# Optimization experiments

Hardware: AMD Instinct MI355X
Metric: run time of the kernel (lower is better)

## Reference

```python
import jax, jax.numpy as jnp
import numpy as np

N = 50000
E = 800000
F_IN = 256
H = 64      # hidden_channels
NH = 4      # GAT heads

def setup_inputs() -> dict:
    key = jax.random.key(0)
    ks = jax.random.split(key, 16)
    x = jax.random.normal(ks[0], (N, F_IN), dtype=jnp.float32)
    edge_index = jax.random.randint(ks[1], (2, E), 0, N, dtype=jnp.int64)
    def w(k, shape, fan_in):
        return jax.random.normal(k, shape, dtype=jnp.float32) / np.sqrt(fan_in)
    return {
        "x": x, "edge_index": edge_index,
        "W1": w(ks[2], (F_IN, H), F_IN), "b1": jnp.zeros((H,), jnp.float32),
        "W2": w(ks[3], (H, H), H),       "b2": jnp.zeros((H,), jnp.float32),
        "Wg": w(ks[4], (H, NH * H), H),
        "att_src": w(ks[5], (NH, H), H), "att_dst": w(ks[6], (NH, H), H),
        "bg": jnp.zeros((NH * H,), jnp.float32),
        "Wf1": w(ks[7], (NH * H, H), NH * H), "bf1": jnp.zeros((H,), jnp.float32),
        "Wf2": w(ks[8], (H, 1), H),           "bf2": jnp.zeros((1,), jnp.float32),
    }

def _with_self_loops(edge_index):
    loops = jnp.arange(N, dtype=edge_index.dtype)
    src = jnp.concatenate([edge_index[0], loops])
    dst = jnp.concatenate([edge_index[1], loops])
    return src, dst

def _gcn(h, src, dst, W, b):
    # h: [N, d_in] -> [N, d_out]; symmetric norm D^-1/2 (A+I) D^-1/2
    h = h @ W
    deg = jax.ops.segment_sum(jnp.ones_like(dst, dtype=h.dtype), dst, num_segments=N)
    dinv = jnp.where(deg > 0, jax.lax.rsqrt(deg), 0.0)
    norm = dinv[src] * dinv[dst]                      # [E2]
    out = jax.ops.segment_sum(h[src] * norm[:, None], dst, num_segments=N)
    return out + b

def _gat(h, src, dst, Wg, att_src, att_dst, bg):
    hp = (h @ Wg).reshape(N, NH, H)                   # [N, NH, H]
    a_src = jnp.einsum('nhd,hd->nh', hp, att_src)     # [N, NH]
    a_dst = jnp.einsum('nhd,hd->nh', hp, att_dst)
    alpha = jax.nn.leaky_relu(a_src[src] + a_dst[dst], negative_slope=0.2)  # [E2, NH]
    amax = jax.ops.segment_max(alpha, dst, num_segments=N)
    e = jnp.exp(alpha - amax[dst])
    denom = jax.ops.segment_sum(e, dst, num_segments=N)
    coef = e / denom[dst]                             # [E2, NH]
    out = jax.ops.segment_sum(hp[src] * coef[:, :, None], dst, num_segments=N)
    return out.reshape(N, NH * H) + bg

def reference(x, edge_index, W1, b1, W2, b2, Wg, att_src, att_dst, bg, Wf1, bf1, Wf2, bf2):
    src, dst = _with_self_loops(edge_index)
    h = jax.nn.relu(_gcn(x, src, dst, W1, b1))        # dropout inactive (eval)
    h = jax.nn.relu(_gcn(h, src, dst, W2, b2))
    h = _gat(h, src, dst, Wg, att_src, att_dst, bg)
    h = jax.nn.relu(h @ Wf1 + bf1)
    return h @ Wf2 + bf2                              # [N, 1]
```

## Files before the change

### kernel.cpp

```cpp
#include <hip/hip_runtime.h>
#include <hip/hip_fp16.h>
#include <math.h>


#define CAP 64
#define CAPSH 6
#define BSH 8
#define NBKT 256
#define BCAP 8192

typedef _Float16 v4h __attribute__((ext_vector_type(4)));
typedef float v4f __attribute__((ext_vector_type(4)));

__device__ __forceinline__ float lrelu02(float a) { return fmaxf(a, 0.2f * a); }

__device__ __forceinline__ float4 lrelu4(float4 a) {
    return make_float4(lrelu02(a.x), lrelu02(a.y), lrelu02(a.z), lrelu02(a.w));
}

__device__ __forceinline__ float4 exp4(float4 a) {
    return make_float4(__expf(a.x), __expf(a.y), __expf(a.z), __expf(a.w));
}

__device__ __forceinline__ float4 unpack4(float2 raw) {
    __half2 h01 = *(__half2*)&raw.x;
    __half2 h23 = *(__half2*)&raw.y;
    float2 f01 = __half22float2(h01);
    float2 f23 = __half22float2(h23);
    return make_float4(f01.x, f01.y, f23.x, f23.y);
}

__device__ __forceinline__ float2 pack4(float4 v) {
    float2 r;
    *(__half2*)&r.x = __float22half2_rn(make_float2(v.x, v.y));
    *(__half2*)&r.y = __float22half2_rn(make_float2(v.z, v.w));
    return r;
}


__launch_bounds__(256)
__global__ void k_bucket(const int* __restrict__ src, const int* __restrict__ dst, int E,
                         int* __restrict__ bcnt, unsigned int* __restrict__ stage) {
    __shared__ int hist[NBKT];
    __shared__ int base[NBKT];
    __shared__ int cur[NBKT];
    int t = threadIdx.x;
    hist[t] = 0; cur[t] = 0;
    __syncthreads();
    int base_e = blockIdx.x * 2048;
    int d[8], s[8];
#pragma unroll
    for (int i = 0; i < 8; i++) {
        int e = base_e + t + i * 256;
        bool ok = (e < E);
        d[i] = ok ? dst[e] : -1;
        s[i] = ok ? src[e] : 0;
        if (ok) atomicAdd(&hist[d[i] >> BSH], 1);
    }
    __syncthreads();
    if (hist[t] > 0) base[t] = atomicAdd(&bcnt[t], hist[t]);
    __syncthreads();
#pragma unroll
    for (int i = 0; i < 8; i++) {
        if (d[i] >= 0) {
            int b = d[i] >> BSH;
            int p = base[b] + atomicAdd(&cur[b], 1);
            if (p < BCAP)
                stage[(size_t)b * BCAP + p] = ((unsigned)d[i] << 16) | (unsigned)s[i];
        }
    }
}


__launch_bounds__(256)
__global__ void k_scatter2(const unsigned int* __restrict__ stage,
                           const int* __restrict__ bcnt, int* __restrict__ cnt,
                           unsigned short* __restrict__ slots, int n) {
    __shared__ int lcnt[1 << BSH];
    int t = threadIdx.x;
    int k = blockIdx.x;
    lcnt[t] = 0;
    __syncthreads();
    int ne = bcnt[k];
    if (ne > BCAP) ne = BCAP;
    const unsigned int* st = stage + (size_t)k * BCAP;
    for (int i = t; i < ne; i += 256) {
        unsigned int e = st[i];
        int d = e >> 16;
        int p = atomicAdd(&lcnt[d & ((1 << BSH) - 1)], 1);
        if (p < CAP) slots[((size_t)d << CAPSH) + p] = (unsigned short)(e & 0xFFFF);
    }
    __syncthreads();
    int v = (k << BSH) + t;
    if (v < n) cnt[v] = lcnt[t];
}


#define GEMM_BODY(BX, K, COLS)                                                     \
    __shared__ float As[16][68];                                                   \
    __shared__ float Bs[16][68];                                                   \
    const int row0 = (BX) * 64;                                                    \
    const int col0 = blockIdx.y * 64;                                              \
    const int t = threadIdx.x;                                                     \
    const int tx = t & 15;                                                         \
    const int ty = t >> 4;                                                         \
    const int lm = t >> 2;                                                         \
    const int lk4 = (t & 3) << 2;                                                  \
    const int wk = t >> 4;                                                         \
    const int wc = (t & 15) << 2;                                                  \
    float acc[4][4] = {};                                                          \
    for (int k0 = 0; k0 < K; k0 += 16) {                                           \
        float4 av = make_float4(0.f, 0.f, 0.f, 0.f);                               \
        int r = row0 + lm;                                                         \
        if (r < nrows) av = *(const float4*)(X + (size_t)r * K + k0 + lk4);        \
        As[lk4 + 0][lm] = av.x;                                                    \
        As[lk4 + 1][lm] = av.y;                                                    \
        As[lk4 + 2][lm] = av.z;                                                    \
        As[lk4 + 3][lm] = av.w;                                                    \
        *(float4*)&Bs[wk][wc] = *(const float4*)(W + (size_t)(k0 + wk) * COLS + col0 + wc); \
        __syncthreads();                                                           \
        _Pragma("unroll") for (int kk = 0; kk < 16; kk++) {                        \
            float4 a = *(const float4*)&As[kk][ty << 2];                           \
            float4 b = *(const float4*)&Bs[kk][tx << 2];                           \
            acc[0][0] = fmaf(a.x, b.x, acc[0][0]);                                 \
            acc[0][1] = fmaf(a.x, b.y, acc[0][1]);                                 \
            acc[0][2] = fmaf(a.x, b.z, acc[0][2]);                                 \
            acc[0][3] = fmaf(a.x, b.w, acc[0][3]);                                 \
            acc[1][0] = fmaf(a.y, b.x, acc[1][0]);                                 \
            acc[1][1] = fmaf(a.y, b.y, acc[1][1]);                                 \
            acc[1][2] = fmaf(a.y, b.z, acc[1][2]);                                 \
            acc[1][3] = fmaf(a.y, b.w, acc[1][3]);                                 \
            acc[2][0] = fmaf(a.z, b.x, acc[2][0]);                                 \
            acc[2][1] = fmaf(a.z, b.y, acc[2][1]);                                 \
            acc[2][2] = fmaf(a.z, b.z, acc[2][2]);                                 \
            acc[2][3] = fmaf(a.z, b.w, acc[2][3]);                                 \
            acc[3][0] = fmaf(a.w, b.x, acc[3][0]);                                 \
            acc[3][1] = fmaf(a.w, b.y, acc[3][1]);                                 \
            acc[3][2] = fmaf(a.w, b.z, acc[3][2]);                                 \
            acc[3][3] = fmaf(a.w, b.w, acc[3][3]);                                 \
        }                                                                          \
        __syncthreads();                                                           \
    }

__launch_bounds__(256)
__global__ void k_fused1(const int* __restrict__ cnt,
                         const float* __restrict__ X, const float* __restrict__ W,
                         __half* __restrict__ Y, int nrows, int gemmBlocks,
                         const float* __restrict__ Wg, const float* __restrict__ att_src,
                         const float* __restrict__ att_dst, const float* __restrict__ Wf1,
                         const float* __restrict__ bf1, const float* __restrict__ bg,
                         const float* __restrict__ W2, float* __restrict__ watt,
                         __half* __restrict__ WcF, __half* __restrict__ W2F,
                         float* __restrict__ bias2) {
    if ((int)blockIdx.x >= gemmBlocks) {
        int b2 = blockIdx.x - gemmBlocks;
        int tt = threadIdx.x;
        if (b2 < 64) {
            int idx = b2 * 256 + tt;
            int r = idx >> 6, c = idx & 63;
            int h = r >> 6, k = r & 63;
            float s = 0.f;
            for (int j = 0; j < 64; j++)
                s = fmaf(Wg[k * 256 + h * 64 + j], Wf1[(h * 64 + j) * 64 + c], s);
            int ks = r >> 4, kr = r & 15;
            int lfrag = ((kr >> 2) << 4) | (c & 15);
            int jf = kr & 3;
            int w = c >> 4;
            WcF[((((w << 4) | ks) << 6) | lfrag) * 4 + jf] = __float2half_rn(s);
        } else {
            for (int idx = tt; idx < 512; idx += 256) {
                int k = idx >> 3, c8 = idx & 7;
                int h = c8 & 3;
                const float* att = (c8 < 4) ? att_src : att_dst;
                float s = 0.f;
                for (int c = 0; c < 64; c++)
                    s = fmaf(Wg[k * 256 + h * 64 + c], att[h * 64 + c], s);
                watt[k * 8 + c8] = s;
            }
            if (tt < 64) {
                float s = bf1[tt];
                for (int j = 0; j < 256; j++) s = fmaf(bg[j], Wf1[j * 64 + tt], s);
                bias2[tt] = s;
            }
            for (int f = tt; f < 4096; f += 256) {
                int jf = f & 3, lfrag = (f >> 2) & 63, ws = f >> 8;
                int w = ws >> 2, ks = ws & 3;
                int k = ks * 16 + ((lfrag >> 4) << 2) + jf;
                int c = w * 16 + (lfrag & 15);
                W2F[f] = __float2half_rn(W2[k * 64 + c]);
            }
        }
        return;
    }
    GEMM_BODY(blockIdx.x, 256, 64)
#pragma unroll
    for (int i = 0; i < 4; i++) {
        int row = row0 + (ty << 2) + i;
        if (row >= nrows) break;
        float dv = rsqrtf((float)(min(cnt[row], CAP) + 1));
        float4 o = make_float4(acc[i][0] * dv, acc[i][1] * dv,
                               acc[i][2] * dv, acc[i][3] * dv);
        ((float2*)(Y + (size_t)row * 64))[tx] = pack4(o);
    }
}


__launch_bounds__(256)
__global__ void k_gcn1_gemm2(const __half* __restrict__ A, const unsigned short* __restrict__ slots,
                             const int* __restrict__ cnt, const float* __restrict__ b1,
                             const __half* __restrict__ W2F, __half* __restrict__ A2, int n) {
    __shared__ alignas(16) __half s_oh[16 * 68];
    __shared__ alignas(16) __half s_res[16 * 68];
    __shared__ float s_dv[16];
    int t = threadIdx.x;
    int lane = t & 63;
    int l = t & 15;
    int nb = t >> 4;
    int v = blockIdx.x * 16 + nb;
    bool act = (v < n);
    if (act) {
        int deg = min(cnt[v], CAP);
        const unsigned short* lst = slots + ((size_t)v << CAPSH);
        float dv = rsqrtf((float)(deg + 1));
        float4 a0 = unpack4(((const float2*)(A + (size_t)v * 64))[l]);
        float4 a1 = make_float4(0.f, 0.f, 0.f, 0.f);
        float4 a2 = a1, a3 = a1;
        int j = 0;
        for (; j + 7 < deg; j += 8) {
            ushort4 sa = *(const ushort4*)(lst + j);
            ushort4 sb = *(const ushort4*)(lst + j + 4);
            float4 t0 = unpack4(((const float2*)(A + (size_t)sa.x * 64))[l]);
            float4 t1 = unpack4(((const float2*)(A + (size_t)sa.y * 64))[l]);
            float4 t2 = unpack4(((const float2*)(A + (size_t)sa.z * 64))[l]);
            float4 t3 = unpack4(((const float2*)(A + (size_t)sa.w * 64))[l]);
            float4 t4 = unpack4(((const float2*)(A + (size_t)sb.x * 64))[l]);
            float4 t5 = unpack4(((const float2*)(A + (size_t)sb.y * 64))[l]);
            float4 t6 = unpack4(((const float2*)(A + (size_t)sb.z * 64))[l]);
            float4 t7 = unpack4(((const float2*)(A + (size_t)sb.w * 64))[l]);
            a0.x += t0.x + t4.x; a0.y += t0.y + t4.y; a0.z += t0.z + t4.z; a0.w += t0.w + t4.w;
            a1.x += t1.x + t5.x; a1.y += t1.y + t5.y; a1.z += t1.z + t5.z; a1.w += t1.w + t5.w;
            a2.x += t2.x + t6.x; a2.y += t2.y + t6.y; a2.z += t2.z + t6.z; a2.w += t2.w + t6.w;
            a3.x += t3.x + t7.x; a3.y += t3.y + t7.y; a3.z += t3.z + t7.z; a3.w += t3.w + t7.w;
        }
        for (; j + 3 < deg; j += 4) {
            ushort4 sa = *(const ushort4*)(lst + j);
            float4 t0 = unpack4(((const float2*)(A + (size_t)sa.x * 64))[l]);
            float4 t1 = unpack4(((const float2*)(A + (size_t)sa.y * 64))[l]);
            float4 t2 = unpack4(((const float2*)(A + (size_t)sa.z * 64))[l]);
            float4 t3 = unpack4(((const float2*)(A + (size_t)sa.w * 64))[l]);
            a0.x += t0.x; a0.y += t0.y; a0.z += t0.z; a0.w += t0.w;
            a1.x += t1.x; a1.y += t1.y; a1.z += t1.z; a1.w += t1.w;
            a2.x += t2.x; a2.y += t2.y; a2.z += t2.z; a2.w += t2.w;
            a3.x += t3.x; a3.y += t3.y; a3.z += t3.z; a3.w += t3.w;
        }
        for (; j < deg; j++) {
            float4 ta = unpack4(((const float2*)(A + (size_t)lst[j] * 64))[l]);
            a0.x += ta.x; a0.y += ta.y; a0.z += ta.z; a0.w += ta.w;
        }
        a0.x += a1.x + a2.x + a3.x;
        a0.y += a1.y + a2.y + a3.y;
        a0.z += a1.z + a2.z + a3.z;
        a0.w += a1.w + a2.w + a3.w;
        float4 b = ((const float4*)b1)[l];
        float4 o;
        o.x = fmaxf(fmaf(dv, a0.x, b.x), 0.f);
        o.y = fmaxf(fmaf(dv, a0.y, b.y), 0.f);
        o.z = fmaxf(fmaf(dv, a0.z, b.z), 0.f);
        o.w = fmaxf(fmaf(dv, a0.w, b.w), 0.f);
        *(float2*)&s_oh[nb * 68 + (l << 2)] = pack4(o);
        if (l == 0) s_dv[nb] = dv;
    } else {
        *(float2*)&s_oh[nb * 68 + (l << 2)] = make_float2(0.f, 0.f);
        if (l == 0) s_dv[nb] = 0.f;
    }
    __syncthreads();
    int w = t >> 6;
    v4f acc = {0.f, 0.f, 0.f, 0.f};
    int arow = (lane & 15) * 68;
    int acol = (lane >> 4) << 2;
#pragma unroll
    for (int ks = 0; ks < 4; ks++) {
        v4h a = *(const v4h*)&s_oh[arow + ks * 16 + acol];
        v4h bfr = *(const v4h*)&W2F[((((w << 2) | ks) << 6) | lane) << 2];
        acc = __builtin_amdgcn_mfma_f32_16x16x16f16(a, bfr, acc, 0, 0, 0);
    }
    int cc = (w << 4) | (lane & 15);
    int m0 = (lane >> 4) << 2;
#pragma unroll
    for (int j = 0; j < 4; j++)
        s_res[(m0 + j) * 68 + cc] = __float2half_rn(acc[j] * s_dv[m0 + j]);
    __syncthreads();
    if (act)
        ((float2*)(A2 + (size_t)v * 64))[l] = *(const float2*)&s_res[nb * 68 + (l << 2)];
}


__launch_bounds__(256)
__global__ void k_gcn2_att(const __half* __restrict__ T, const unsigned short* __restrict__ slots,
                           const int* __restrict__ cnt, const float* __restrict__ bias,
                           const float* __restrict__ watt, __half* __restrict__ Out,
                           float* __restrict__ asrc, float* __restrict__ adst, int n) {
    int t = threadIdx.x;
    int l = t & 15;
    int v = blockIdx.x * 16 + (t >> 4);
    if (v >= n) return;
    int deg = min(cnt[v], CAP);
    const unsigned short* lst = slots + ((size_t)v << CAPSH);
    float dv = rsqrtf((float)(deg + 1));
    float4 a0 = unpack4(((const float2*)(T + (size_t)v * 64))[l]);
    float4 a1 = make_float4(0.f, 0.f, 0.f, 0.f);
    float4 a2 = a1, a3 = a1;
    int j = 0;
    for (; j + 7 < deg; j += 8) {
        ushort4 sa = *(const ushort4*)(lst + j);
        ushort4 sb = *(const ushort4*)(lst + j + 4);
        float4 t0 = unpack4(((const float2*)(T + (size_t)sa.x * 64))[l]);
        float4 t1 = unpack4(((const float2*)(T + (size_t)sa.y * 64))[l]);
        float4 t2 = unpack4(((const float2*)(T + (size_t)sa.z * 64))[l]);
        float4 t3 = unpack4(((const float2*)(T + (size_t)sa.w * 64))[l]);
        float4 t4 = unpack4(((const float2*)(T + (size_t)sb.x * 64))[l]);
        float4 t5 = unpack4(((const float2*)(T + (size_t)sb.y * 64))[l]);
        float4 t6 = unpack4(((const float2*)(T + (size_t)sb.z * 64))[l]);
        float4 t7 = unpack4(((const float2*)(T + (size_t)sb.w * 64))[l]);
        a0.x += t0.x + t4.x; a0.y += t0.y + t4.y; a0.z += t0.z + t4.z; a0.w += t0.w + t4.w;
        a1.x += t1.x + t5.x; a1.y += t1.y + t5.y; a1.z += t1.z + t5.z; a1.w += t1.w + t5.w;
        a2.x += t2.x + t6.x; a2.y += t2.y + t6.y; a2.z += t2.z + t6.z; a2.w += t2.w + t6.w;
        a3.x += t3.x + t7.x; a3.y += t3.y + t7.y; a3.z += t3.z + t7.z; a3.w += t3.w + t7.w;
    }
    for (; j + 3 < deg; j += 4) {
        ushort4 sa = *(const ushort4*)(lst + j);
        float4 t0 = unpack4(((const float2*)(T + (size_t)sa.x * 64))[l]);
        float4 t1 = unpack4(((const float2*)(T + (size_t)sa.y * 64))[l]);
        float4 t2 = unpack4(((const float2*)(T + (size_t)sa.z * 64))[l]);
        float4 t3 = unpack4(((const float2*)(T + (size_t)sa.w * 64))[l]);
        a0.x += t0.x; a0.y += t0.y; a0.z += t0.z; a0.w += t0.w;
        a1.x += t1.x; a1.y += t1.y; a1.z += t1.z; a1.w += t1.w;
        a2.x += t2.x; a2.y += t2.y; a2.z += t2.z; a2.w += t2.w;
        a3.x += t3.x; a3.y += t3.y; a3.z += t3.z; a3.w += t3.w;
    }
    for (; j < deg; j++) {
        float4 ta = unpack4(((const float2*)(T + (size_t)lst[j] * 64))[l]);
        a0.x += ta.x; a0.y += ta.y; a0.z += ta.z; a0.w += ta.w;
    }
    a0.x += a1.x + a2.x + a3.x;
    a0.y += a1.y + a2.y + a3.y;
    a0.z += a1.z + a2.z + a3.z;
    a0.w += a1.w + a2.w + a3.w;
    float4 b = ((const float4*)bias)[l];
    float4 o;
    o.x = fmaxf(fmaf(dv, a0.x, b.x), 0.f);
    o.y = fmaxf(fmaf(dv, a0.y, b.y), 0.f);
    o.z = fmaxf(fmaf(dv, a0.z, b.z), 0.f);
    o.w = fmaxf(fmaf(dv, a0.w, b.w), 0.f);
    ((float2*)(Out + (size_t)v * 64))[l] = pack4(o);
    const float* wr = watt + (l << 2) * 8;
    float4 w0a = *(const float4*)(wr +  0), w0b = *(const float4*)(wr +  4);
    float4 w1a = *(const float4*)(wr +  8), w1b = *(const float4*)(wr + 12);
    float4 w2a = *(const float4*)(wr + 16), w2b = *(const float4*)(wr + 20);
    float4 w3a = *(const float4*)(wr + 24), w3b = *(const float4*)(wr + 28);
    float4 ds, dd;
    ds.x = o.x*w0a.x + o.y*w1a.x + o.z*w2a.x + o.w*w3a.x;
    ds.y = o.x*w0a.y + o.y*w1a.y + o.z*w2a.y + o.w*w3a.y;
    ds.z = o.x*w0a.z + o.y*w1a.z + o.z*w2a.z + o.w*w3a.z;
    ds.w = o.x*w0a.w + o.y*w1a.w + o.z*w2a.w + o.w*w3a.w;
    dd.x = o.x*w0b.x + o.y*w1b.x + o.z*w2b.x + o.w*w3b.x;
    dd.y = o.x*w0b.y + o.y*w1b.y + o.z*w2b.y + o.w*w3b.y;
    dd.z = o.x*w0b.z + o.y*w1b.z + o.z*w2b.z + o.w*w3b.z;
    dd.w = o.x*w0b.w + o.y*w1b.w + o.z*w2b.w + o.w*w3b.w;
    for (int off = 1; off <= 8; off <<= 1) {
        ds.x += __shfl_xor(ds.x, off); ds.y += __shfl_xor(ds.y, off);
        ds.z += __shfl_xor(ds.z, off); ds.w += __shfl_xor(ds.w, off);
        dd.x += __shfl_xor(dd.x, off); dd.y += __shfl_xor(dd.y, off);
        dd.z += __shfl_xor(dd.z, off); dd.w += __shfl_xor(dd.w, off);
    }
    if (l == 0) {
        ((float4*)asrc)[v] = ds;
        ((float4*)adst)[v] = dd;
    }
}


__launch_bounds__(256)
__global__ void k_gat_head(const __half* __restrict__ Bt, const unsigned short* __restrict__ slots,
                           const int* __restrict__ cnt, const float* __restrict__ asrc,
                           const float* __restrict__ adst, const __half* __restrict__ WcF,
                           const float* __restrict__ bias2, const float* __restrict__ Wf2,
                           const float* __restrict__ bf2, float* __restrict__ out, int n) {
    __shared__ alignas(16) __half s_aggh[16 * 260];
    __shared__ alignas(16) float s_e[16 * 68];
    __shared__ int s_sidx[16 * 17];
    __shared__ float s_part[16][4];
    int t = threadIdx.x;
    int lane = t & 63;
    int l = lane & 15;
    int nb = t >> 4;
    int v = blockIdx.x * 16 + nb;
    bool act = (v < n);
    if (act) {
        int deg = min(cnt[v], CAP);
        const unsigned short* lst = slots + ((size_t)v << CAPSH);
        float4 ad4 = ((const float4*)adst)[v];
        float4 as4 = ((const float4*)asrc)[v];
        float4 es = exp4(lrelu4(make_float4(as4.x + ad4.x, as4.y + ad4.y,
                                            as4.z + ad4.z, as4.w + ad4.w)));
        float4 esum = (l == 0) ? es : make_float4(0.f, 0.f, 0.f, 0.f);
        float4 bv = unpack4(((const float2*)(Bt + (size_t)v * 64))[l]);
        float4 acc0 = make_float4(es.x * bv.x, es.x * bv.y, es.x * bv.z, es.x * bv.w);
        float4 acc1 = make_float4(es.y * bv.x, es.y * bv.y, es.y * bv.z, es.y * bv.w);
        float4 acc2 = make_float4(es.z * bv.x, es.z * bv.y, es.z * bv.z, es.z * bv.w);
        float4 acc3 = make_float4(es.w * bv.x, es.w * bv.y, es.w * bv.z, es.w * bv.w);
        for (int c0 = 0; c0 < deg; c0 += 16) {
            int cl = min(16, deg - c0);
            float4 e = make_float4(0.f, 0.f, 0.f, 0.f);
            if (l < cl) {
                int s = lst[c0 + l];
                float4 sa = ((const float4*)asrc)[s];
                e = exp4(lrelu4(make_float4(sa.x + ad4.x, sa.y + ad4.y,
                                            sa.z + ad4.z, sa.w + ad4.w)));
                esum.x += e.x; esum.y += e.y; esum.z += e.z; esum.w += e.w;
                s_sidx[nb * 17 + l] = s;
            }
            *(float4*)&s_e[nb * 68 + (l << 2)] = e;
            __builtin_amdgcn_sched_barrier(0);
            for (int jj = 0; jj < cl; jj++) {
                int so = s_sidx[nb * 17 + jj];
                float4 ev = *(const float4*)&s_e[nb * 68 + (jj << 2)];
                float4 tv = unpack4(((const float2*)(Bt + (size_t)so * 64))[l]);
                acc0.x = fmaf(ev.x, tv.x, acc0.x); acc0.y = fmaf(ev.x, tv.y, acc0.y);
                acc0.z = fmaf(ev.x, tv.z, acc0.z); acc0.w = fmaf(ev.x, tv.w, acc0.w);
                acc1.x = fmaf(ev.y, tv.x, acc1.x); acc1.y = fmaf(ev.y, tv.y, acc1.y);
                acc1.z = fmaf(ev.y, tv.z, acc1.z); acc1.w = fmaf(ev.y, tv.w, acc1.w);
                acc2.x = fmaf(ev.z, tv.x, acc2.x); acc2.y = fmaf(ev.z, tv.y, acc2.y);
                acc2.z = fmaf(ev.z, tv.z, acc2.z); acc2.w = fmaf(ev.z, tv.w, acc2.w);
                acc3.x = fmaf(ev.w, tv.x, acc3.x); acc3.y = fmaf(ev.w, tv.y, acc3.y);
                acc3.z = fmaf(ev.w, tv.z, acc3.z); acc3.w = fmaf(ev.w, tv.w, acc3.w);
            }
        }
        for (int o = 8; o >= 1; o >>= 1) {
            esum.x += __shfl_xor(esum.x, o); esum.y += __shfl_xor(esum.y, o);
            esum.z += __shfl_xor(esum.z, o); esum.w += __shfl_xor(esum.w, o);
        }
        float i0 = 1.f / esum.x, i1 = 1.f / esum.y, i2 = 1.f / esum.z, i3 = 1.f / esum.w;
        *(float2*)&s_aggh[nb * 260 +   0 + (l << 2)] =
            pack4(make_float4(acc0.x*i0, acc0.y*i0, acc0.z*i0, acc0.w*i0));
        *(float2*)&s_aggh[nb * 260 +  64 + (l << 2)] =
            pack4(make_float4(acc1.x*i1, acc1.y*i1, acc1.z*i1, acc1.w*i1));
        *(float2*)&s_aggh[nb * 260 + 128 + (l << 2)] =
            pack4(make_float4(acc2.x*i2, acc2.y*i2, acc2.z*i2, acc2.w*i2));
        *(float2*)&s_aggh[nb * 260 + 192 + (l << 2)] =
            pack4(make_float4(acc3.x*i3, acc3.y*i3, acc3.z*i3, acc3.w*i3));
    } else {
        float2 z = make_float2(0.f, 0.f);
        *(float2*)&s_aggh[nb * 260 +   0 + (l << 2)] = z;
        *(float2*)&s_aggh[nb * 260 +  64 + (l << 2)] = z;
        *(float2*)&s_aggh[nb * 260 + 128 + (l << 2)] = z;
        *(float2*)&s_aggh[nb * 260 + 192 + (l << 2)] = z;
    }
    __syncthreads();
    int w = t >> 6;
    v4f accA = {0.f, 0.f, 0.f, 0.f};
    v4f accB = {0.f, 0.f, 0.f, 0.f};
    int arow = l * 260;
    int acol = (lane >> 4) << 2;
#pragma unroll
    for (int ks = 0; ks < 16; ks += 2) {
        v4h a0f = *(const v4h*)&s_aggh[arow + ks * 16 + acol];
        v4h b0f = *(const v4h*)&WcF[((((w << 4) | ks) << 6) | lane) << 2];
        accA = __builtin_amdgcn_mfma_f32_16x16x16f16(a0f, b0f, accA, 0, 0, 0);
        v4h a1f = *(const v4h*)&s_aggh[arow + (ks + 1) * 16 + acol];
        v4h b1f = *(const v4h*)&WcF[((((w << 4) | (ks + 1)) << 6) | lane) << 2];
        accB = __builtin_amdgcn_mfma_f32_16x16x16f16(a1f, b1f, accB, 0, 0, 0);
    }
    int cc = (w << 4) | l;
    float bb = bias2[cc], wq = Wf2[cc];
    float p0 = fmaxf(accA[0] + accB[0] + bb, 0.f) * wq;
    float p1 = fmaxf(accA[1] + accB[1] + bb, 0.f) * wq;
    float p2 = fmaxf(accA[2] + accB[2] + bb, 0.f) * wq;
    float p3 = fmaxf(accA[3] + accB[3] + bb, 0.f) * wq;
    for (int o = 1; o <= 8; o <<= 1) {
        p0 += __shfl_xor(p0, o); p1 += __shfl_xor(p1, o);
        p2 += __shfl_xor(p2, o); p3 += __shfl_xor(p3, o);
    }
    if (l == 0) {
        int m0 = (lane >> 4) << 2;
        s_part[m0 + 0][w] = p0; s_part[m0 + 1][w] = p1;
        s_part[m0 + 2][w] = p2; s_part[m0 + 3][w] = p3;
    }
    __syncthreads();
    if (t < 16 && blockIdx.x * 16 + t < n)
        out[blockIdx.x * 16 + t] =
            s_part[t][0] + s_part[t][1] + s_part[t][2] + s_part[t][3] + bf2[0];
}


extern "C" void kernel_launch(void* const* d_in, const int* in_sizes, int n_in,
                              void* d_out, int out_size, void* d_ws, size_t ws_size,
                              hipStream_t stream) {
    const float* x       = (const float*)d_in[0];
    const int*   ei      = (const int*)d_in[1];
    const float* W1      = (const float*)d_in[2];
    const float* b1      = (const float*)d_in[3];
    const float* W2      = (const float*)d_in[4];
    const float* b2      = (const float*)d_in[5];
    const float* Wg      = (const float*)d_in[6];
    const float* att_src = (const float*)d_in[7];
    const float* att_dst = (const float*)d_in[8];
    const float* bg      = (const float*)d_in[9];
    const float* Wf1     = (const float*)d_in[10];
    const float* bf1     = (const float*)d_in[11];
    const float* Wf2     = (const float*)d_in[12];
    const float* bf2     = (const float*)d_in[13];
    float* out = (float*)d_out;

    const int N = in_sizes[0] / 256;
    const int E = in_sizes[1] / 2;
    const int* src = ei;
    const int* dst = ei + E;

    char* p = (char*)d_ws;
    auto alloc = [&](size_t bytes) {
        void* r = (void*)p;
        p += (bytes + 255) & ~(size_t)255;
        return r;
    };
    __half* A   = (__half*)alloc((size_t)N * 64 * 2);
    __half* A2  = (__half*)alloc((size_t)N * 64 * 2);
    __half* B   = (__half*)alloc((size_t)N * 64 * 2);
    float* asrc = (float*)alloc((size_t)N * 4 * 4);
    float* adst = (float*)alloc((size_t)N * 4 * 4);
    int*   cnt  = (int*)alloc((size_t)N * 4);
    unsigned short* slots = (unsigned short*)alloc((size_t)N * CAP * 2);
    int* bcnt = (int*)alloc(NBKT * 4);
    unsigned int* stage = (unsigned int*)alloc((size_t)NBKT * BCAP * 4);
    float* watt   = (float*)alloc(64 * 8 * 4);
    __half* WcF   = (__half*)alloc(256 * 64 * 2);
    __half* W2F   = (__half*)alloc(64 * 64 * 2);
    float* bias2  = (float*)alloc(64 * 4);

    const int gBkt = (E + 2047) / 2048;
    const int nbused = (N + (1 << BSH) - 1) >> BSH;
    const int grow = (N + 63) / 64;
    const int gagg = (N + 15) / 16;

    hipMemsetAsync(bcnt, 0, NBKT * 4, stream);

    k_bucket<<<gBkt, 256, 0, stream>>>(src, dst, E, bcnt, stage);

    k_scatter2<<<nbused, 256, 0, stream>>>(stage, bcnt, cnt, slots, N);

    k_fused1<<<grow + 65, 256, 0, stream>>>(
        cnt, x, W1, A, N, grow,
        Wg, att_src, att_dst, Wf1, bf1, bg, W2, watt, WcF, W2F, bias2);

    k_gcn1_gemm2<<<gagg, 256, 0, stream>>>(A, slots, cnt, b1, W2F, A2, N);

    k_gcn2_att<<<gagg, 256, 0, stream>>>(A2, slots, cnt, b2, watt, B, asrc, adst, N);

    k_gat_head<<<gagg, 256, 0, stream>>>(B, slots, cnt, asrc, adst,
                                         WcF, bias2, Wf2, bf2, out, N);
}
```

Before: 237.7 us.

## Replace FP32 SIMT first-layer GEMM with fp16 MFMA using prepacked W1 fragments

The first GCN linear layer (X @ W1, 50000x256x64) moves from a scalar FP32 shared-memory tiled GEMM to MFMA 16x16x16 fp16 instructions. W1 is converted to fp16 and laid out in MFMA B-fragment order by one extra block added to the bucketing kernel. X tiles are converted to fp16 in shared memory, and results go through a shared-memory staging buffer for coalesced 16-byte stores. The aim is to cut compute time in this GEMM, which is likely bound by reading the 51 MB X. Rounding X and W1 to fp16 lowers input precision.

Result: faster. 225.3 us (-5.2%).

```diff
diff --git a/kernel.cpp b/kernel.cpp
--- a/kernel.cpp
+++ b/kernel.cpp
@@ -40,7 +40,19 @@
 
 __launch_bounds__(256)
 __global__ void k_bucket(const int* __restrict__ src, const int* __restrict__ dst, int E,
-                         int* __restrict__ bcnt, unsigned int* __restrict__ stage) {
+                         int* __restrict__ bcnt, unsigned int* __restrict__ stage,
+                         int nBktBlocks, const float* __restrict__ W1,
+                         __half* __restrict__ W1F) {
+    if ((int)blockIdx.x >= nBktBlocks) {
+        for (int f = threadIdx.x; f < 16384; f += 256) {
+            int jf = f & 3, lane = (f >> 2) & 63, ws = f >> 8;
+            int w = ws >> 4, ks = ws & 15;
+            int k = ks * 16 + ((lane >> 4) << 2) + jf;
+            int c = (w << 4) | (lane & 15);
+            W1F[f] = __float2half_rn(W1[k * 64 + c]);
+        }
+        return;
+    }
     __shared__ int hist[NBKT];
     __shared__ int base[NBKT];
     __shared__ int cur[NBKT];
@@ -96,55 +108,9 @@
 }
 
 
-#define GEMM_BODY(BX, K, COLS)                                                     \
-    __shared__ float As[16][68];                                                   \
-    __shared__ float Bs[16][68];                                                   \
-    const int row0 = (BX) * 64;                                                    \
-    const int col0 = blockIdx.y * 64;                                              \
-    const int t = threadIdx.x;                                                     \
-    const int tx = t & 15;                                                         \
-    const int ty = t >> 4;                                                         \
-    const int lm = t >> 2;                                                         \
-    const int lk4 = (t & 3) << 2;                                                  \
-    const int wk = t >> 4;                                                         \
-    const int wc = (t & 15) << 2;                                                  \
-    float acc[4][4] = {};                                                          \
-    for (int k0 = 0; k0 < K; k0 += 16) {                                           \
-        float4 av = make_float4(0.f, 0.f, 0.f, 0.f);                               \
-        int r = row0 + lm;                                                         \
-        if (r < nrows) av = *(const float4*)(X + (size_t)r * K + k0 + lk4);        \
-        As[lk4 + 0][lm] = av.x;                                                    \
-        As[lk4 + 1][lm] = av.y;                                                    \
-        As[lk4 + 2][lm] = av.z;                                                    \
-        As[lk4 + 3][lm] = av.w;                                                    \
-        *(float4*)&Bs[wk][wc] = *(const float4*)(W + (size_t)(k0 + wk) * COLS + col0 + wc); \
-        __syncthreads();                                                           \
-        _Pragma("unroll") for (int kk = 0; kk < 16; kk++) {                        \
-            float4 a = *(const float4*)&As[kk][ty << 2];                           \
-            float4 b = *(const float4*)&Bs[kk][tx << 2];                           \
-            acc[0][0] = fmaf(a.x, b.x, acc[0][0]);                                 \
-            acc[0][1] = fmaf(a.x, b.y, acc[0][1]);                                 \
-            acc[0][2] = fmaf(a.x, b.z, acc[0][2]);                                 \
-            acc[0][3] = fmaf(a.x, b.w, acc[0][3]);                                 \
-            acc[1][0] = fmaf(a.y, b.x, acc[1][0]);                                 \
-            acc[1][1] = fmaf(a.y, b.y, acc[1][1]);                                 \
-            acc[1][2] = fmaf(a.y, b.z, acc[1][2]);                                 \
-            acc[1][3] = fmaf(a.y, b.w, acc[1][3]);                                 \
-            acc[2][0] = fmaf(a.z, b.x, acc[2][0]);                                 \
-            acc[2][1] = fmaf(a.z, b.y, acc[2][1]);                                 \
-            acc[2][2] = fmaf(a.z, b.z, acc[2][2]);                                 \
-            acc[2][3] = fmaf(a.z, b.w, acc[2][3]);                                 \
-            acc[3][0] = fmaf(a.w, b.x, acc[3][0]);                                 \
-            acc[3][1] = fmaf(a.w, b.y, acc[3][1]);                                 \
-            acc[3][2] = fmaf(a.w, b.z, acc[3][2]);                                 \
-            acc[3][3] = fmaf(a.w, b.w, acc[3][3]);                                 \
-        }                                                                          \
-        __syncthreads();                                                           \
-    }
-
 __launch_bounds__(256)
 __global__ void k_fused1(const int* __restrict__ cnt,
-                         const float* __restrict__ X, const float* __restrict__ W,
+                         const float* __restrict__ X, const __half* __restrict__ W1F,
                          __half* __restrict__ Y, int nrows, int gemmBlocks,
                          const float* __restrict__ Wg, const float* __restrict__ att_src,
                          const float* __restrict__ att_dst, const float* __restrict__ Wf1,
@@ -192,15 +158,70 @@
         }
         return;
     }
-    GEMM_BODY(blockIdx.x, 256, 64)
-#pragma unroll
-    for (int i = 0; i < 4; i++) {
-        int row = row0 + (ty << 2) + i;
-        if (row >= nrows) break;
-        float dv = rsqrtf((float)(min(cnt[row], CAP) + 1));
-        float4 o = make_float4(acc[i][0] * dv, acc[i][1] * dv,
-                               acc[i][2] * dv, acc[i][3] * dv);
-        ((float2*)(Y + (size_t)row * 64))[tx] = pack4(o);
+    __shared__ alignas(16) __half s_a[64 * 40];
+    __shared__ alignas(16) __half s_res[64 * 72];
+    __shared__ float s_dv[64];
+    const int row0 = blockIdx.x * 64;
+    const int t = threadIdx.x;
+    const int lane = t & 63;
+    const int w = t >> 6;
+    if (t < 64) {
+        int r = row0 + t;
+        s_dv[t] = (r < nrows) ? rsqrtf((float)(min(cnt[r], CAP) + 1)) : 0.f;
+    }
+    const int srow = t >> 2;
+    const int scg  = (t & 3) << 3;
+    const int am = lane & 15;
+    const int ak = (lane >> 4) << 2;
+    v4f acc0 = {0.f, 0.f, 0.f, 0.f};
+    v4f acc1 = acc0, acc2 = acc0, acc3 = acc0;
+    for (int kc = 0; kc < 8; kc++) {
+        float4 xa = make_float4(0.f, 0.f, 0.f, 0.f);
+        float4 xb = xa;
+        int rr = row0 + srow;
+        if (rr < nrows) {
+            const float* xp = X + (size_t)rr * 256 + kc * 32 + scg;
+            xa = *(const float4*)(xp);
+            xb = *(const float4*)(xp + 4);
+        }
+        float2 lo = pack4(xa), hi = pack4(xb);
+        *(float4*)&s_a[srow * 40 + scg] = make_float4(lo.x, lo.y, hi.x, hi.y);
+        __syncthreads();
+        int ks0 = kc << 1;
+        v4h b0 = *(const v4h*)&W1F[((((w << 4) | ks0) << 6) | lane) << 2];
+        v4h b1 = *(const v4h*)&W1F[((((w << 4) | (ks0 + 1)) << 6) | lane) << 2];
+#pragma unroll
+        for (int half = 0; half < 2; half++) {
+            v4h b = half ? b1 : b0;
+            int co = (half << 4) + ak;
+            acc0 = __builtin_amdgcn_mfma_f32_16x16x16f16(
+                       *(const v4h*)&s_a[(am) * 40 + co], b, acc0, 0, 0, 0);
+            acc1 = __builtin_amdgcn_mfma_f32_16x16x16f16(
+                       *(const v4h*)&s_a[(16 + am) * 40 + co], b, acc1, 0, 0, 0);
+            acc2 = __builtin_amdgcn_mfma_f32_16x16x16f16(
+                       *(const v4h*)&s_a[(32 + am) * 40 + co], b, acc2, 0, 0, 0);
+            acc3 = __builtin_amdgcn_mfma_f32_16x16x16f16(
+                       *(const v4h*)&s_a[(48 + am) * 40 + co], b, acc3, 0, 0, 0);
+        }
+        __syncthreads();
+    }
+    int cc = (w << 4) | am;
+#pragma unroll
+    for (int j = 0; j < 4; j++) {
+        int m = ak + j;
+        s_res[(m) * 72 + cc]      = __float2half_rn(acc0[j] * s_dv[m]);
+        s_res[(16 + m) * 72 + cc] = __float2half_rn(acc1[j] * s_dv[16 + m]);
+        s_res[(32 + m) * 72 + cc] = __float2half_rn(acc2[j] * s_dv[32 + m]);
+        s_res[(48 + m) * 72 + cc] = __float2half_rn(acc3[j] * s_dv[48 + m]);
+    }
+    __syncthreads();
+#pragma unroll
+    for (int i = 0; i < 2; i++) {
+        int idx = t + i * 256;
+        int row = idx >> 3, c8 = (idx & 7) << 3;
+        int rr = row0 + row;
+        if (rr < nrows)
+            *(float4*)(Y + (size_t)rr * 64 + c8) = *(const float4*)&s_res[row * 72 + c8];
     }
 }
 
@@ -535,6 +556,7 @@
     float* watt   = (float*)alloc(64 * 8 * 4);
     __half* WcF   = (__half*)alloc(256 * 64 * 2);
     __half* W2F   = (__half*)alloc(64 * 64 * 2);
+    __half* W1F   = (__half*)alloc(256 * 64 * 2);
     float* bias2  = (float*)alloc(64 * 4);
 
     const int gBkt = (E + 2047) / 2048;
@@ -544,12 +566,12 @@
 
     hipMemsetAsync(bcnt, 0, NBKT * 4, stream);
 
-    k_bucket<<<gBkt, 256, 0, stream>>>(src, dst, E, bcnt, stage);
+    k_bucket<<<gBkt + 1, 256, 0, stream>>>(src, dst, E, bcnt, stage, gBkt, W1, W1F);
 
     k_scatter2<<<nbused, 256, 0, stream>>>(stage, bcnt, cnt, slots, N);
 
     k_fused1<<<grow + 65, 256, 0, stream>>>(
-        cnt, x, W1, A, N, grow,
+        cnt, x, W1F, A, N, grow,
         Wg, att_src, att_dst, Wf1, bf1, bg, W2, watt, WcF, W2F, bias2);
 
     k_gcn1_gemm2<<<gagg, 256, 0, stream>>>(A, slots, cnt, b1, W2F, A2, N);
```
